# Performance work log

Measured on AMD Instinct MI355X. Metric: run time of the kernel, lower is better.

The kernel has to match this reference:

```python
import jax, jax.numpy as jnp
import numpy as np

# --- GridEncoder config (matches torch-ngp defaults) ---
D = 3                 # input_dim
L = 16                # num_levels
C = 2                 # level_dim
H = 16                # base_resolution
PLS = 2.0             # per_level_scale
LOG2_HASHMAP = 19
MAX_PARAMS = 2 ** LOG2_HASHMAP
PRIMES = (1, 2654435761, 805459861)  # fast_hash primes for D=3
ALIGN_CORNERS = False


def _level_meta():
    """Replicates the offsets computation in GridEncoder.__init__ and the
    kernel's per-level resolution / hash-vs-dense decision."""
    metas = []
    off = 0
    for l in range(L):
        res = int(np.ceil(H * PLS ** l))            # kernel: ceil(exp2(l*S)*H - 1) + 1 == H*2^l here
        full = (res if ALIGN_CORNERS else res + 1) ** D
        params = min(MAX_PARAMS, full)
        params = int(np.ceil(params / 8) * 8)       # pad to multiple of 8
        hashed = full > params                      # kernel: stride > hashmap_size after index loop
        metas.append((off, params, res, hashed))
        off += params
    return metas, off

METAS, TOTAL_PARAMS = _level_meta()


def setup_inputs() -> dict:
    key = jax.random.key(0)
    k1, k2 = jax.random.split(key)
    B = 1048576
    inputs = jax.random.uniform(k1, (B, D), dtype=jnp.float32, minval=-1.0, maxval=1.0)
    # reset_parameters(): uniform(-1e-4, 1e-4)
    embeddings = jax.random.uniform(k2, (TOTAL_PARAMS, C), dtype=jnp.float32,
                                    minval=-1e-4, maxval=1e-4)
    return {"inputs": inputs, "embeddings": embeddings}


def _grid_encode(x, embeddings):
    """x: [B, D] in [0, 1]. Returns [B, L*C]."""
    corner_bits = jnp.array([[(c >> d) & 1 for d in range(D)] for c in range(2 ** D)],
                            dtype=jnp.uint32)                       # [8, D]
    primes = jnp.array(PRIMES, dtype=jnp.uint32)
    outs = []
    for l, (off, size, res, hashed) in enumerate(METAS):
        scale = float(np.exp2(l) * H - 1.0)                          # exp2(l*S)*H - 1, S = log2(2) = 1
        pos = x * scale + (0.0 if ALIGN_CORNERS else 0.5)            # [B, D]
        pg_f = jnp.floor(pos)
        frac = pos - pg_f                                            # [B, D] linear interp weights
        pg = pg_f.astype(jnp.uint32)                                 # [B, D]
        corners = pg[None, :, :] + corner_bits[:, None, :]           # [8, B, D]
        # N-linear interpolation weights: prod over dims of frac / (1-frac)
        w = jnp.prod(jnp.where(corner_bits[:, None, :] == 1,
                               frac[None, :, :], 1.0 - frac[None, :, :]), axis=-1)  # [8, B]
        if hashed:
            # fast_hash: xor of pos_grid[d] * primes[d] in wrapping uint32
            idx = corners[..., 0] * primes[0]
            for d in range(1, D):
                idx = idx ^ (corners[..., d] * primes[d])
        else:
            base = res if ALIGN_CORNERS else res + 1
            stride = jnp.array([base ** d for d in range(D)], dtype=jnp.uint32)
            idx = (corners * stride).sum(axis=-1).astype(jnp.uint32)
        idx = (idx % jnp.uint32(size)) + jnp.uint32(off)             # [8, B]
        emb = embeddings[idx]                                        # [8, B, C] gather
        outs.append(jnp.einsum('kb,kbc->bc', w, emb))                # [B, C]
    return jnp.concatenate(outs, axis=-1)                            # [B, L*C], level-major


def reference(inputs, embeddings):
    bound = 1.0
    x = (inputs + bound) / (2.0 * bound)   # map to [0, 1]
    return _grid_encode(x, embeddings)
```

## Files before the change

kernel.cpp:

```cpp
#include <hip/hip_runtime.h>
#include <cstdint>


namespace {

using f32x2 = __attribute__((ext_vector_type(2))) float;
using f32x4 = __attribute__((ext_vector_type(4))) float;

__device__ __forceinline__ void level_setup(
    float x, float y, float z, uint32_t l,
    uint32_t idx[8], float w[8]) {
  uint32_t res = 16u << l;
  float scale = (float)res - 1.0f;

  float px = x * scale + 0.5f;
  float py = y * scale + 0.5f;
  float pz = z * scale + 0.5f;
  float gx = floorf(px), gy = floorf(py), gz = floorf(pz);
  float rx = px - gx, ry = py - gy, rz = pz - gz;
  uint32_t ix = (uint32_t)gx, iy = (uint32_t)gy, iz = (uint32_t)gz;

  uint32_t off = (l >= 3u) ? (l * 524288u - 1257368u)
                           : ((l == 0u) ? 0u : ((l == 1u) ? 4920u : 40864u));
  bool hashed = (l >= 3u);

  uint32_t base = res + 1u;
  uint32_t bb = base * base;
  const uint32_t P2 = 2654435761u, P3 = 805459861u;

  uint32_t dy0 = iy * base, dy1 = dy0 + base;
  uint32_t dz0 = iz * bb,   dz1 = dz0 + bb;
  uint32_t hy0 = iy * P2,   hy1 = hy0 + P2;
  uint32_t hz0 = iz * P3,   hz1 = hz0 + P3;

#pragma unroll
  for (int c = 0; c < 8; ++c) {
    uint32_t cx = ix + (uint32_t)(c & 1);
    uint32_t h = (cx ^ ((c & 2) ? hy1 : hy0) ^ ((c & 4) ? hz1 : hz0)) & 0x7FFFFu;
    uint32_t d = cx + ((c & 2) ? dy1 : dy0) + ((c & 4) ? dz1 : dz0);
    idx[c] = (hashed ? h : d) + off;
  }

  float wx1 = rx, wx0 = 1.0f - rx;
  float wy1 = ry, wy0 = 1.0f - ry;
  float wz1 = rz, wz0 = 1.0f - rz;
#pragma unroll
  for (int c = 0; c < 8; ++c) {
    w[c] = ((c & 1) ? wx1 : wx0) *
           ((c & 2) ? wy1 : wy0) *
           ((c & 4) ? wz1 : wz0);
  }
}

__global__ __launch_bounds__(256) void gather_lm_kernel(
    const float* __restrict__ in,
    const f32x2* __restrict__ emb,
    f32x2* __restrict__ ws,
    uint32_t B) {
  uint32_t l = blockIdx.y;
  uint32_t p = blockIdx.x * 256u + threadIdx.x;
  if (p >= B) return;

  float x = (__builtin_nontemporal_load(&in[p * 3 + 0]) + 1.0f) * 0.5f;
  float y = (__builtin_nontemporal_load(&in[p * 3 + 1]) + 1.0f) * 0.5f;
  float z = (__builtin_nontemporal_load(&in[p * 3 + 2]) + 1.0f) * 0.5f;

  uint32_t res = 16u << l;
  float scale = (float)res - 1.0f;
  float px = x * scale + 0.5f;
  float py = y * scale + 0.5f;
  float pz = z * scale + 0.5f;
  float gx = floorf(px), gy = floorf(py), gz = floorf(pz);
  float rx = px - gx, ry = py - gy, rz = pz - gz;
  uint32_t ix = (uint32_t)gx, iy = (uint32_t)gy, iz = (uint32_t)gz;

  f32x2 e[8];

  if (l >= 3u) {
    uint32_t off = l * 524288u - 1257368u;
    const f32x2* __restrict__ tab = emb + off;
    const uint32_t P2 = 2654435761u, P3 = 805459861u;
    uint32_t hy0 = iy * P2, hy1 = hy0 + P2;
    uint32_t hz0 = iz * P3, hz1 = hz0 + P3;
    uint32_t hb0 = hy0 ^ hz0, hb1 = hy1 ^ hz0, hb2 = hy0 ^ hz1, hb3 = hy1 ^ hz1;
    uint32_t hb[4] = {hb0, hb1, hb2, hb3};

    if ((ix & 1u) == 0u) {
#pragma unroll
      for (int j = 0; j < 4; ++j) {
        uint32_t h0 = (ix ^ hb[j]) & 0x7FFFFu;
        f32x4 v = *reinterpret_cast<const f32x4*>(tab + (h0 & ~1u));
        f32x2 lo; lo.x = v.x; lo.y = v.y;
        f32x2 hi; hi.x = v.z; hi.y = v.w;
        bool swap = (h0 & 1u) != 0u;
        e[2 * j]     = swap ? hi : lo;
        e[2 * j + 1] = swap ? lo : hi;
      }
    } else {
      uint32_t ix1 = ix + 1u;
#pragma unroll
      for (int j = 0; j < 4; ++j) {
        e[2 * j]     = tab[(ix  ^ hb[j]) & 0x7FFFFu];
        e[2 * j + 1] = tab[(ix1 ^ hb[j]) & 0x7FFFFu];
      }
    }
  } else {
    uint32_t off = (l == 0u) ? 0u : ((l == 1u) ? 4920u : 40864u);
    uint32_t base = res + 1u;
    uint32_t bb = base * base;
    uint32_t dy0 = iy * base, dy1 = dy0 + base;
    uint32_t dz0 = iz * bb,   dz1 = dz0 + bb;
#pragma unroll
    for (int c = 0; c < 8; ++c) {
      uint32_t cx = ix + (uint32_t)(c & 1);
      uint32_t d = cx + ((c & 2) ? dy1 : dy0) + ((c & 4) ? dz1 : dz0);
      e[c] = emb[d + off];
    }
  }

  float wx1 = rx, wx0 = 1.0f - rx;
  float wy1 = ry, wy0 = 1.0f - ry;
  float wz1 = rz, wz0 = 1.0f - rz;

  float o0 = 0.0f, o1 = 0.0f;
#pragma unroll
  for (int c = 0; c < 8; ++c) {
    float w = ((c & 1) ? wx1 : wx0) *
              ((c & 2) ? wy1 : wy0) *
              ((c & 4) ? wz1 : wz0);
    o0 = fmaf(w, e[c].x, o0);
    o1 = fmaf(w, e[c].y, o1);
  }

  f32x2 r; r.x = o0; r.y = o1;
  __builtin_nontemporal_store(r, &ws[(size_t)l * B + p]);
}

__global__ __launch_bounds__(256) void transpose_kernel(
    const f32x2* __restrict__ ws,
    f32x4* __restrict__ out,
    uint32_t B) {
  uint32_t t = blockIdx.x * 256u + threadIdx.x;
  if (t >= B * 8u) return;
  uint32_t j = t & 7u;
  uint32_t q = t >> 3;
  f32x2 a = __builtin_nontemporal_load(&ws[(size_t)(2u * j)      * B + q]);
  f32x2 b = __builtin_nontemporal_load(&ws[(size_t)(2u * j + 1u) * B + q]);
  f32x4 v; v.x = a.x; v.y = a.y; v.z = b.x; v.w = b.y;
  __builtin_nontemporal_store(v, &out[t]);
}

__global__ __launch_bounds__(256) void grid_encode_fallback(
    const float* __restrict__ in, const f32x2* __restrict__ emb,
    f32x4* __restrict__ out, uint32_t B) {
  uint32_t p = blockIdx.x * 256u + threadIdx.x;
  if (p >= B) return;
  float x = (in[p * 3 + 0] + 1.0f) * 0.5f;
  float y = (in[p * 3 + 1] + 1.0f) * 0.5f;
  float z = (in[p * 3 + 2] + 1.0f) * 0.5f;
#pragma unroll 1
  for (uint32_t l = 0; l < 16u; l += 2u) {
    uint32_t ia[8], ib[8]; float wa[8], wb[8];
    level_setup(x, y, z, l, ia, wa);
    level_setup(x, y, z, l + 1u, ib, wb);
    f32x2 ea[8], eb[8];
#pragma unroll
    for (int c = 0; c < 8; ++c) ea[c] = emb[ia[c]];
#pragma unroll
    for (int c = 0; c < 8; ++c) eb[c] = emb[ib[c]];
    float a0 = 0, a1 = 0, b0 = 0, b1 = 0;
#pragma unroll
    for (int c = 0; c < 8; ++c) {
      a0 = fmaf(wa[c], ea[c].x, a0);
      a1 = fmaf(wa[c], ea[c].y, a1);
      b0 = fmaf(wb[c], eb[c].x, b0);
      b1 = fmaf(wb[c], eb[c].y, b1);
    }
    f32x4 v; v.x = a0; v.y = a1; v.z = b0; v.w = b1;
    out[(size_t)p * 8u + (l >> 1)] = v;
  }
}

}

extern "C" void kernel_launch(void* const* d_in, const int* in_sizes, int n_in,
                              void* d_out, int out_size, void* d_ws, size_t ws_size,
                              hipStream_t stream) {
  (void)n_in; (void)out_size;
  const float* in = (const float*)d_in[0];
  const f32x2* emb = (const f32x2*)d_in[1];
  f32x4* out = (f32x4*)d_out;
  uint32_t B = (uint32_t)(in_sizes[0] / 3);
  uint32_t pblocks = (B + 255u) / 256u;

  size_t ws_needed = (size_t)16 * B * sizeof(f32x2);
  if (ws_size >= ws_needed) {
    f32x2* ws = (f32x2*)d_ws;
    hipLaunchKernelGGL(gather_lm_kernel, dim3(pblocks, 16), dim3(256), 0,
                       stream, in, emb, ws, B);
    uint32_t tblocks = (B * 8u + 255u) / 256u;
    hipLaunchKernelGGL(transpose_kernel, dim3(tblocks), dim3(256), 0,
                       stream, ws, out, B);
  } else {
    hipLaunchKernelGGL(grid_encode_fallback, dim3(pblocks), dim3(256), 0,
                       stream, in, emb, out, B);
  }
}
```

Measured before the change: 608.6 us.

## Gather all corners as aligned 16B pair loads and keep workspace cache-resident

Every corner fetch, dense or hashed, now loads the aligned 16-byte pair that holds the entry and picks the right half. This replaces the old parity-dependent split between 8-byte loads and pair loads, which made lanes diverge. Workspace writes and transpose reads drop the nontemporal hint so the intermediate can stay in L2/MALL. The transpose handles two outputs per thread. The cost is fetching twice the bytes per corner for odd-parity and dense lookups, and the fallback is rewritten to go one level at a time.

```diff
diff --git a/kernel.cpp b/kernel.cpp
--- a/kernel.cpp
+++ b/kernel.cpp
@@ -7,48 +7,31 @@
 using f32x2 = __attribute__((ext_vector_type(2))) float;
 using f32x4 = __attribute__((ext_vector_type(4))) float;
 
-__device__ __forceinline__ void level_setup(
-    float x, float y, float z, uint32_t l,
-    uint32_t idx[8], float w[8]) {
-  uint32_t res = 16u << l;
-  float scale = (float)res - 1.0f;
-
-  float px = x * scale + 0.5f;
-  float py = y * scale + 0.5f;
-  float pz = z * scale + 0.5f;
-  float gx = floorf(px), gy = floorf(py), gz = floorf(pz);
-  float rx = px - gx, ry = py - gy, rz = pz - gz;
-  uint32_t ix = (uint32_t)gx, iy = (uint32_t)gy, iz = (uint32_t)gz;
-
-  uint32_t off = (l >= 3u) ? (l * 524288u - 1257368u)
-                           : ((l == 0u) ? 0u : ((l == 1u) ? 4920u : 40864u));
-  bool hashed = (l >= 3u);
-
-  uint32_t base = res + 1u;
-  uint32_t bb = base * base;
-  const uint32_t P2 = 2654435761u, P3 = 805459861u;
-
-  uint32_t dy0 = iy * base, dy1 = dy0 + base;
-  uint32_t dz0 = iz * bb,   dz1 = dz0 + bb;
-  uint32_t hy0 = iy * P2,   hy1 = hy0 + P2;
-  uint32_t hz0 = iz * P3,   hz1 = hz0 + P3;
-
+__device__ __forceinline__ void level_indices(
+    uint32_t ix, uint32_t iy, uint32_t iz, uint32_t l, uint32_t g[8]) {
+  if (l >= 3u) {
+    uint32_t off = l * 524288u - 1257368u;
+    const uint32_t P2 = 2654435761u, P3 = 805459861u;
+    uint32_t hy0 = iy * P2, hy1 = hy0 + P2;
+    uint32_t hz0 = iz * P3, hz1 = hz0 + P3;
+    uint32_t hb[4] = {hy0 ^ hz0, hy1 ^ hz0, hy0 ^ hz1, hy1 ^ hz1};
+    uint32_t ix1 = ix + 1u;
 #pragma unroll
-  for (int c = 0; c < 8; ++c) {
-    uint32_t cx = ix + (uint32_t)(c & 1);
-    uint32_t h = (cx ^ ((c & 2) ? hy1 : hy0) ^ ((c & 4) ? hz1 : hz0)) & 0x7FFFFu;
-    uint32_t d = cx + ((c & 2) ? dy1 : dy0) + ((c & 4) ? dz1 : dz0);
-    idx[c] = (hashed ? h : d) + off;
-  }
-
-  float wx1 = rx, wx0 = 1.0f - rx;
-  float wy1 = ry, wy0 = 1.0f - ry;
-  float wz1 = rz, wz0 = 1.0f - rz;
+    for (int j = 0; j < 4; ++j) {
+      g[2 * j]     = ((ix  ^ hb[j]) & 0x7FFFFu) + off;
+      g[2 * j + 1] = ((ix1 ^ hb[j]) & 0x7FFFFu) + off;
+    }
+  } else {
+    uint32_t off = (l == 0u) ? 0u : ((l == 1u) ? 4920u : 40864u);
+    uint32_t base = (16u << l) + 1u;
+    uint32_t bb = base * base;
+    uint32_t dy0 = iy * base, dy1 = dy0 + base;
+    uint32_t dz0 = iz * bb,   dz1 = dz0 + bb;
 #pragma unroll
-  for (int c = 0; c < 8; ++c) {
-    w[c] = ((c & 1) ? wx1 : wx0) *
-           ((c & 2) ? wy1 : wy0) *
-           ((c & 4) ? wz1 : wz0);
+    for (int c = 0; c < 8; ++c) {
+      g[c] = ix + (uint32_t)(c & 1) +
+             ((c & 2) ? dy1 : dy0) + ((c & 4) ? dz1 : dz0) + off;
+    }
   }
 }
 
@@ -74,48 +57,17 @@
   float rx = px - gx, ry = py - gy, rz = pz - gz;
   uint32_t ix = (uint32_t)gx, iy = (uint32_t)gy, iz = (uint32_t)gz;
 
+  uint32_t g[8];
+  level_indices(ix, iy, iz, l, g);
+
+  const f32x4* __restrict__ pr = reinterpret_cast<const f32x4*>(emb);
   f32x2 e[8];
-
-  if (l >= 3u) {
-    uint32_t off = l * 524288u - 1257368u;
-    const f32x2* __restrict__ tab = emb + off;
-    const uint32_t P2 = 2654435761u, P3 = 805459861u;
-    uint32_t hy0 = iy * P2, hy1 = hy0 + P2;
-    uint32_t hz0 = iz * P3, hz1 = hz0 + P3;
-    uint32_t hb0 = hy0 ^ hz0, hb1 = hy1 ^ hz0, hb2 = hy0 ^ hz1, hb3 = hy1 ^ hz1;
-    uint32_t hb[4] = {hb0, hb1, hb2, hb3};
-
-    if ((ix & 1u) == 0u) {
 #pragma unroll
-      for (int j = 0; j < 4; ++j) {
-        uint32_t h0 = (ix ^ hb[j]) & 0x7FFFFu;
-        f32x4 v = *reinterpret_cast<const f32x4*>(tab + (h0 & ~1u));
-        f32x2 lo; lo.x = v.x; lo.y = v.y;
-        f32x2 hi; hi.x = v.z; hi.y = v.w;
-        bool swap = (h0 & 1u) != 0u;
-        e[2 * j]     = swap ? hi : lo;
-        e[2 * j + 1] = swap ? lo : hi;
-      }
-    } else {
-      uint32_t ix1 = ix + 1u;
-#pragma unroll
-      for (int j = 0; j < 4; ++j) {
-        e[2 * j]     = tab[(ix  ^ hb[j]) & 0x7FFFFu];
-        e[2 * j + 1] = tab[(ix1 ^ hb[j]) & 0x7FFFFu];
-      }
-    }
-  } else {
-    uint32_t off = (l == 0u) ? 0u : ((l == 1u) ? 4920u : 40864u);
-    uint32_t base = res + 1u;
-    uint32_t bb = base * base;
-    uint32_t dy0 = iy * base, dy1 = dy0 + base;
-    uint32_t dz0 = iz * bb,   dz1 = dz0 + bb;
-#pragma unroll
-    for (int c = 0; c < 8; ++c) {
-      uint32_t cx = ix + (uint32_t)(c & 1);
-      uint32_t d = cx + ((c & 2) ? dy1 : dy0) + ((c & 4) ? dz1 : dz0);
-      e[c] = emb[d + off];
-    }
+  for (int c = 0; c < 8; ++c) {
+    f32x4 v = pr[g[c] >> 1];
+    f32x2 lo; lo.x = v.x; lo.y = v.y;
+    f32x2 hi; hi.x = v.z; hi.y = v.w;
+    e[c] = (g[c] & 1u) ? hi : lo;
   }
 
   float wx1 = rx, wx0 = 1.0f - rx;
@@ -133,21 +85,29 @@
   }
 
   f32x2 r; r.x = o0; r.y = o1;
-  __builtin_nontemporal_store(r, &ws[(size_t)l * B + p]);
+  ws[(size_t)l * B + p] = r;
 }
 
 __global__ __launch_bounds__(256) void transpose_kernel(
     const f32x2* __restrict__ ws,
     f32x4* __restrict__ out,
     uint32_t B) {
+  uint32_t half = B * 4u;
   uint32_t t = blockIdx.x * 256u + threadIdx.x;
-  if (t >= B * 8u) return;
-  uint32_t j = t & 7u;
-  uint32_t q = t >> 3;
-  f32x2 a = __builtin_nontemporal_load(&ws[(size_t)(2u * j)      * B + q]);
-  f32x2 b = __builtin_nontemporal_load(&ws[(size_t)(2u * j + 1u) * B + q]);
-  f32x4 v; v.x = a.x; v.y = a.y; v.z = b.x; v.w = b.y;
-  __builtin_nontemporal_store(v, &out[t]);
+  if (t >= half) return;
+  uint32_t o0 = t, o1 = t + half;
+  uint32_t j0 = o0 & 7u, q0 = o0 >> 3;
+  uint32_t j1 = o1 & 7u, q1 = o1 >> 3;
+
+  f32x2 a0 = ws[(size_t)(2u * j0)      * B + q0];
+  f32x2 b0 = ws[(size_t)(2u * j0 + 1u) * B + q0];
+  f32x2 a1 = ws[(size_t)(2u * j1)      * B + q1];
+  f32x2 b1 = ws[(size_t)(2u * j1 + 1u) * B + q1];
+
+  f32x4 v0; v0.x = a0.x; v0.y = a0.y; v0.z = b0.x; v0.w = b0.y;
+  f32x4 v1; v1.x = a1.x; v1.y = a1.y; v1.z = b1.x; v1.w = b1.y;
+  __builtin_nontemporal_store(v0, &out[o0]);
+  __builtin_nontemporal_store(v1, &out[o1]);
 }
 
 __global__ __launch_bounds__(256) void grid_encode_fallback(
@@ -158,26 +118,41 @@
   float x = (in[p * 3 + 0] + 1.0f) * 0.5f;
   float y = (in[p * 3 + 1] + 1.0f) * 0.5f;
   float z = (in[p * 3 + 2] + 1.0f) * 0.5f;
+  const f32x4* __restrict__ pr = reinterpret_cast<const f32x4*>(emb);
 #pragma unroll 1
-  for (uint32_t l = 0; l < 16u; l += 2u) {
-    uint32_t ia[8], ib[8]; float wa[8], wb[8];
-    level_setup(x, y, z, l, ia, wa);
-    level_setup(x, y, z, l + 1u, ib, wb);
-    f32x2 ea[8], eb[8];
-#pragma unroll
-    for (int c = 0; c < 8; ++c) ea[c] = emb[ia[c]];
-#pragma unroll
-    for (int c = 0; c < 8; ++c) eb[c] = emb[ib[c]];
-    float a0 = 0, a1 = 0, b0 = 0, b1 = 0;
+  for (uint32_t l = 0; l < 16u; ++l) {
+    uint32_t res = 16u << l;
+    float scale = (float)res - 1.0f;
+    float px = x * scale + 0.5f;
+    float py = y * scale + 0.5f;
+    float pz = z * scale + 0.5f;
+    float gx = floorf(px), gy = floorf(py), gz = floorf(pz);
+    float rx = px - gx, ry = py - gy, rz = pz - gz;
+    uint32_t ix = (uint32_t)gx, iy = (uint32_t)gy, iz = (uint32_t)gz;
+    uint32_t g[8];
+    level_indices(ix, iy, iz, l, g);
+    f32x2 e[8];
 #pragma unroll
     for (int c = 0; c < 8; ++c) {
-      a0 = fmaf(wa[c], ea[c].x, a0);
-      a1 = fmaf(wa[c], ea[c].y, a1);
-      b0 = fmaf(wb[c], eb[c].x, b0);
-      b1 = fmaf(wb[c], eb[c].y, b1);
+      f32x4 v = pr[g[c] >> 1];
+      f32x2 lo; lo.x = v.x; lo.y = v.y;
+      f32x2 hi; hi.x = v.z; hi.y = v.w;
+      e[c] = (g[c] & 1u) ? hi : lo;
     }
-    f32x4 v; v.x = a0; v.y = a1; v.z = b0; v.w = b1;
-    out[(size_t)p * 8u + (l >> 1)] = v;
+    float wx1 = rx, wx0 = 1.0f - rx;
+    float wy1 = ry, wy0 = 1.0f - ry;
+    float wz1 = rz, wz0 = 1.0f - rz;
+    float o0 = 0.0f, o1 = 0.0f;
+#pragma unroll
+    for (int c = 0; c < 8; ++c) {
+      float w = ((c & 1) ? wx1 : wx0) *
+                ((c & 2) ? wy1 : wy0) *
+                ((c & 4) ? wz1 : wz0);
+      o0 = fmaf(w, e[c].x, o0);
+      o1 = fmaf(w, e[c].y, o1);
+    }
+    f32x2 r; r.x = o0; r.y = o1;
+    reinterpret_cast<f32x2*>(out)[(size_t)p * 16u + l] = r;
   }
 }
 
@@ -198,7 +173,7 @@
     f32x2* ws = (f32x2*)d_ws;
     hipLaunchKernelGGL(gather_lm_kernel, dim3(pblocks, 16), dim3(256), 0,
                        stream, in, emb, ws, B);
-    uint32_t tblocks = (B * 8u + 255u) / 256u;
+    uint32_t tblocks = (B * 4u + 255u) / 256u;
     hipLaunchKernelGGL(transpose_kernel, dim3(tblocks), dim3(256), 0,
                        stream, ws, out, B);
   } else {
```

After: 754.5 us. 1.24x slower.
